# Performance work log

Hardware: AMD Instinct MI355X
Metric: run time of the kernel (lower is better)

Reference implementation:

```python
import jax, jax.numpy as jnp
import numpy as np

CODE_NUM = 12288
GRAPH = 128      # graph_size: embedding width / GRU input
HIDDEN = 128     # GRU hidden = t_output_size = time_size (required by scatter/broadcast)
ATT = 64         # t_attention_size


def setup_inputs() -> dict:
    key = jax.random.key(0)
    ks = jax.random.split(key, 20)
    s = 0.05
    # disjoint 3-way membership masks (m1/m2/m3), some codes in no set
    cat = jax.random.randint(ks[0], (CODE_NUM,), 0, 4)
    divided = jax.nn.one_hot(cat, 4, dtype=jnp.int32)[:, :3]
    return {
        "interval": jnp.asarray(3.5, jnp.float32),
        "co_embeddings": jax.random.normal(ks[1], (CODE_NUM, GRAPH), jnp.float32),
        "no_embeddings": jax.random.normal(ks[2], (CODE_NUM, GRAPH), jnp.float32),
        "unrelated_embeddings": jax.random.normal(ks[3], (CODE_NUM, GRAPH), jnp.float32),
        "hidden_state": jax.random.normal(ks[4], (CODE_NUM, HIDDEN), jnp.float32),
        "divided": divided,
        # GRUCell params (torch layout: [3H, in], gates r|z|n)
        "W_ih": jax.random.normal(ks[5], (3 * HIDDEN, GRAPH), jnp.float32) * s,
        "W_hh": jax.random.normal(ks[6], (3 * HIDDEN, HIDDEN), jnp.float32) * s,
        "b_ih": jax.random.normal(ks[7], (3 * HIDDEN,), jnp.float32) * s,
        "b_hh": jax.random.normal(ks[8], (3 * HIDDEN,), jnp.float32) * s,
        # SingleHeadAttentionLayer params
        "Wq": jax.random.normal(ks[9], (ATT, GRAPH), jnp.float32) * s,
        "bq": jax.random.normal(ks[10], (ATT,), jnp.float32) * s,
        "Wk": jax.random.normal(ks[11], (ATT, GRAPH), jnp.float32) * s,
        "bk": jax.random.normal(ks[12], (ATT,), jnp.float32) * s,
        "Wv": jax.random.normal(ks[13], (HIDDEN, GRAPH), jnp.float32) * s,
        "bv": jax.random.normal(ks[14], (HIDDEN,), jnp.float32) * s,
        # time_layer: Linear(1, time_size)
        "Wt": jax.random.normal(ks[15], (HIDDEN, 1), jnp.float32) * s,
        "bt": jax.random.normal(ks[16], (HIDDEN,), jnp.float32) * s,
        "t": 1,
        "is_last": 0,
    }


def _gru_cell(x, h, W_ih, W_hh, b_ih, b_hh):
    gi = x @ W_ih.T + b_ih          # [N, 3H]
    gh = h @ W_hh.T + b_hh          # [N, 3H]
    i_r, i_z, i_n = jnp.split(gi, 3, axis=-1)
    h_r, h_z, h_n = jnp.split(gh, 3, axis=-1)
    r = jax.nn.sigmoid(i_r + h_r)
    z = jax.nn.sigmoid(i_z + h_z)
    n = jnp.tanh(i_n + r * h_n)
    return (1.0 - z) * n + z * h


def reference(interval, co_embeddings, no_embeddings, unrelated_embeddings,
              hidden_state, divided, W_ih, W_hh, b_ih, b_hh,
              Wq, bq, Wk, bk, Wv, bv, Wt, bt, t, is_last):
    dt = co_embeddings.dtype
    # time feature: tanh(Linear(1/log(interval + e)))
    x_t = 1.0 / jnp.log(interval + jnp.e)                       # scalar
    time_features = jnp.tanh(x_t * Wt[:, 0] + bt)               # [H]

    if is_last:
        out = _gru_cell(co_embeddings, hidden_state, W_ih, W_hh, b_ih, b_hh)
        return (out + time_features, None)

    m1 = divided[:, 0] > 0
    m2 = divided[:, 1] > 0
    m3 = divided[:, 2] > 0
    m23 = m2 | m3
    NEG = jnp.finfo(dt).min

    # --- m1 branch: GRUCell is row-wise, so compute on all rows and mask ---
    h_gru = _gru_cell(co_embeddings, hidden_state, W_ih, W_hh, b_ih, b_hh)  # [N, H]
    output_m1 = jnp.max(jnp.where(m1[:, None], h_gru, NEG), axis=0)        # [H]

    # --- m2/m3 branch: attention over the m23 subset (mask-based, order-free)
    # query rows: m2 -> no_embeddings, m3 -> unrelated_embeddings
    q_full = jnp.where(m2[:, None], no_embeddings, unrelated_embeddings)   # [N, G]
    Q = q_full @ Wq.T + bq                                                 # [N, A]
    K = co_embeddings @ Wk.T + bk                                          # [N, A]
    V = co_embeddings @ Wv.T + bv                                          # [N, H]
    scores = (Q @ K.T) / jnp.sqrt(jnp.asarray(ATT, dt))                    # [N, N]
    scores = jnp.where(m23[None, :], scores, NEG)                          # keys restricted to m23
    attn = jax.nn.softmax(scores, axis=-1)
    h_att = jnp.tanh(attn @ V)                                             # [N, H]
    output_m23 = jnp.max(jnp.where(m23[:, None], h_att, NEG), axis=0)      # [H]

    # scatter: m2/m3 rows written after m1 rows (m23 takes precedence)
    h_new = jnp.where(m23[:, None], h_att,
                      jnp.where(m1[:, None], h_gru, jnp.zeros((), dt)))

    output = jnp.maximum(output_m1, output_m23)
    return (output + time_features, h_new)
```

## Files before the change

### kernel.cpp

```cpp
#include <hip/hip_runtime.h>
#include <hip/hip_bf16.h>
#include <math.h>

#define N_CODES 12288
#define G 128
#define H 128
#define ATT 64
#define NEGF (-3.4028234663852886e38f)
#define NSEG 8
#define QT 64
#define QMAX 7168
#define NQTA (QMAX / QT)

typedef __attribute__((ext_vector_type(8))) short bf16x8;
typedef __attribute__((ext_vector_type(4))) float f32x4;
typedef __hip_bfloat16 bf16;
#define MFMA16(a, b, c) __builtin_amdgcn_mfma_f32_16x16x32_bf16(a, b, c, 0, 0, 0)

struct __align__(16) Ws {
  int n1;
  int n23;
  int cnt;
  int pad_;
  int idx1[N_CODES];
  int rows23[N_CODES];
  int flags23[N_CODES];
  unsigned maxu[128];
  float tf[128];
  float lseg[NSEG * QMAX];
  float bqkv[256];
  float b2[512];
  bf16 Wqkv[16 * 4 * 64 * 8];
  bf16 W2[32 * 8 * 64 * 8];
  bf16 Qb[(size_t)N_CODES * ATT];
  bf16 Kf[(size_t)N_CODES * ATT];
  bf16 Vf[(size_t)N_CODES * H];
  bf16 Oseg[(size_t)NSEG * QMAX * H];
};

__device__ inline uint2 pack4(float4 v) {
  union { bf16 b[4]; uint2 u; } cv;
  cv.b[0] = __float2bfloat16(v.x);
  cv.b[1] = __float2bfloat16(v.y);
  cv.b[2] = __float2bfloat16(v.z);
  cv.b[3] = __float2bfloat16(v.w);
  return cv.u;
}

__device__ inline float bf2f(short s) {
  union { unsigned u; float f; } c;
  c.u = ((unsigned)(unsigned short)s) << 16;
  return c.f;
}

__device__ inline unsigned fkey(float f) {
  unsigned b = __float_as_uint(f);
  return (b & 0x80000000u) ? ~b : (b | 0x80000000u);
}
__device__ inline float funkey(unsigned u) {
  unsigned b = (u & 0x80000000u) ? (u & 0x7fffffffu) : ~u;
  return __uint_as_float(b);
}

__global__ void k_setup(const int* __restrict__ divided,
                        const float* __restrict__ Wq, const float* __restrict__ bq,
                        const float* __restrict__ Wk, const float* __restrict__ bk,
                        const float* __restrict__ Wv, const float* __restrict__ bv,
                        const float* __restrict__ W_ih, const float* __restrict__ W_hh,
                        const float* __restrict__ b_ih, const float* __restrict__ b_hh,
                        const float* __restrict__ interval, const float* __restrict__ Wt,
                        const float* __restrict__ bt, Ws* ws, float* __restrict__ h_new) {
  int bid = blockIdx.x;
  int t = threadIdx.x;
  if (bid < 48) {
    int r = bid * 256 + t;
    int m1 = divided[r * 3 + 0] > 0;
    int m2 = divided[r * 3 + 1] > 0;
    int m3 = divided[r * 3 + 2] > 0;
    if (m1) {
      int p = atomicAdd(&ws->n1, 1);
      ws->idx1[p] = r;
    }
    if (m2 | m3) {
      int p = atomicAdd(&ws->n23, 1);
      ws->rows23[p] = r;
      ws->flags23[p] = m2;
    }
    if (!(m1 | m2 | m3)) {
      float4 z = {0.f, 0.f, 0.f, 0.f};
      float4* hr = (float4*)&h_new[(size_t)r * H];
#pragma unroll
      for (int i = 0; i < 32; ++i) hr[i] = z;
    }
    return;
  }
  if (bid < 80) {
    int idx = (bid - 48) * 256 + t;
    int c = idx >> 5, k = (idx & 31) * 4;
    float4 v;
    if (c < 64) {
      v = *(const float4*)&Wq[c * G + k];
      v.x *= 0.125f; v.y *= 0.125f; v.z *= 0.125f; v.w *= 0.125f;
    } else if (c < 128) {
      v = *(const float4*)&Wk[(c - 64) * G + k];
    } else {
      v = *(const float4*)&Wv[(c - 128) * G + k];
    }
    int NB = c >> 4, lo = c & 15, ks = k >> 5, hi = (k >> 3) & 3, j = k & 7;
    *(uint2*)&ws->Wqkv[((NB * 4 + ks) * 64 + hi * 16 + lo) * 8 + j] = pack4(v);
    return;
  }
  if (bid < 208) {
    int idx = (bid - 80) * 256 + t;
    int c = idx >> 6, k = (idx & 63) * 4;
    int g = c >> 7, d = c & 127;
    float4 v = {0.f, 0.f, 0.f, 0.f};
    if (g == 0) v = (k < 128) ? *(const float4*)&W_ih[d * G + k]
                              : *(const float4*)&W_hh[d * H + (k - 128)];
    else if (g == 1) v = (k < 128) ? *(const float4*)&W_ih[(128 + d) * G + k]
                                   : *(const float4*)&W_hh[(128 + d) * H + (k - 128)];
    else if (g == 2) { if (k < 128) v = *(const float4*)&W_ih[(256 + d) * G + k]; }
    else { if (k >= 128) v = *(const float4*)&W_hh[(256 + d) * H + (k - 128)]; }
    int NB = c >> 4, lo = c & 15, ks = k >> 5, hi = (k >> 3) & 3, j = k & 7;
    *(uint2*)&ws->W2[((NB * 8 + ks) * 64 + hi * 16 + lo) * 8 + j] = pack4(v);
    return;
  }
  if (t < 128) {
    float xt = 1.0f / logf(interval[0] + 2.718281828459045f);
    ws->tf[t] = tanhf(xt * Wt[t] + bt[t]);
    ws->maxu[t] = 0u;
  }
  for (int i = t; i < 768; i += 256) {
    if (i < 256) {
      float v;
      if (i < 64) v = bq[i] * 0.125f;
      else if (i < 128) v = bk[i - 64];
      else v = bv[i - 128];
      ws->bqkv[i] = v;
    } else {
      int c = i - 256;
      int g = c >> 7, d = c & 127;
      float v;
      if (g == 0) v = b_ih[d] + b_hh[d];
      else if (g == 1) v = b_ih[128 + d] + b_hh[128 + d];
      else if (g == 2) v = b_ih[256 + d];
      else v = b_hh[256 + d];
      ws->b2[c] = v;
    }
  }
}

__launch_bounds__(256)
__global__ void k_mm(const float* __restrict__ co, const float* __restrict__ no_e,
                     const float* __restrict__ un_e, const float* __restrict__ hs,
                     Ws* ws, float* __restrict__ h_new) {
  __shared__ __align__(16) bf16 sm[8704];
  int bid = blockIdx.x;
  int t = threadIdx.x;
  int w = t >> 6, lane = t & 63, lo = lane & 15, hi = lane >> 4;

  if (bid < 448) {
    int n23 = ws->n23;
    int q0 = bid * 16;
    if (q0 >= n23) return;
    bf16(*Aq)[136] = (bf16(*)[136])sm;
    bf16(*Ac)[136] = (bf16(*)[136])(sm + 2176);
    for (int it = 0; it < 2; ++it) {
      int idx = it * 256 + t;
      int rr = idx >> 5, c4 = idx & 31;
      uint2 pq = {0, 0}, pc = {0, 0};
      int p = q0 + rr;
      if (p < n23) {
        int row = ws->rows23[p];
        const float* srcq = ws->flags23[p] ? no_e : un_e;
        pq = pack4(*(const float4*)&srcq[(size_t)row * G + c4 * 4]);
        pc = pack4(*(const float4*)&co[(size_t)row * G + c4 * 4]);
      }
      *(uint2*)&Aq[rr][c4 * 4] = pq;
      *(uint2*)&Ac[rr][c4 * 4] = pc;
    }
    __syncthreads();
    const bf16(*At)[136] = (w == 0) ? Aq : Ac;
    f32x4 acc[4];
#pragma unroll
    for (int nb = 0; nb < 4; ++nb) acc[nb] = (f32x4){0.f, 0.f, 0.f, 0.f};
#pragma unroll
    for (int ks = 0; ks < 4; ++ks) {
      bf16x8 af = *(const bf16x8*)&At[lo][ks * 32 + hi * 8];
#pragma unroll
      for (int nb = 0; nb < 4; ++nb) {
        bf16x8 bfr = *(const bf16x8*)&ws->Wqkv[(((w * 4 + nb) * 4 + ks) * 64 + lane) * 8];
        acc[nb] = MFMA16(af, bfr, acc[nb]);
      }
    }
#pragma unroll
    for (int nb = 0; nb < 4; ++nb) {
      int c = w * 64 + nb * 16 + lo;
      float bias = ws->bqkv[c];
#pragma unroll
      for (int r = 0; r < 4; ++r) {
        int p = q0 + hi * 4 + r;
        if (p >= n23) continue;
        bf16 bv16 = __float2bfloat16(acc[nb][r] + bias);
        if (c < 64) {
          ws->Qb[(size_t)p * ATT + c] = bv16;
        } else if (c < 128) {
          int d = c - 64;
          ws->Kf[(((p >> 4) * 2 + (d >> 5)) * 64 + ((d >> 3) & 3) * 16 + (p & 15)) * 8 + (d & 7)] = bv16;
        } else {
          int d = c - 128;
          ws->Vf[((((p >> 6) * 8 + (d >> 4)) * 2 + ((p >> 5) & 1)) * 64 + ((p >> 3) & 3) * 16 + (d & 15)) * 8 + (p & 7)] = bv16;
        }
      }
    }
  } else {
    int n1 = ws->n1;
    int q0 = (bid - 448) * 16;
    if (q0 >= n1) return;
    bf16(*A2)[264] = (bf16(*)[264])sm;
    for (int it = 0; it < 4; ++it) {
      int idx = it * 256 + t;
      int rr = idx >> 6, c4 = idx & 63;
      uint2 pk = {0, 0};
      int p = q0 + rr;
      if (p < n1) {
        int row = ws->idx1[p];
        float4 v = (c4 < 32) ? *(const float4*)&co[(size_t)row * G + c4 * 4]
                             : *(const float4*)&hs[(size_t)row * H + (c4 - 32) * 4];
        pk = pack4(v);
      }
      *(uint2*)&A2[rr][c4 * 4] = pk;
    }
    __syncthreads();
    f32x4 acc[8];
#pragma unroll
    for (int x = 0; x < 8; ++x) acc[x] = (f32x4){0.f, 0.f, 0.f, 0.f};
#pragma unroll
    for (int ks = 0; ks < 8; ++ks) {
      bf16x8 af = *(const bf16x8*)&A2[lo][ks * 32 + hi * 8];
#pragma unroll
      for (int g = 0; g < 4; ++g) {
#pragma unroll
        for (int nb2 = 0; nb2 < 2; ++nb2) {
          int NB = g * 8 + w * 2 + nb2;
          bf16x8 bfr = *(const bf16x8*)&ws->W2[((NB * 8 + ks) * 64 + lane) * 8];
          acc[g * 2 + nb2] = MFMA16(af, bfr, acc[g * 2 + nb2]);
        }
      }
    }
    float mx2[2] = {NEGF, NEGF};
#pragma unroll
    for (int nb2 = 0; nb2 < 2; ++nb2) {
      int d = w * 32 + nb2 * 16 + lo;
      float br = ws->b2[d], bz = ws->b2[128 + d], bin_ = ws->b2[256 + d], bhn = ws->b2[384 + d];
#pragma unroll
      for (int r = 0; r < 4; ++r) {
        int p = q0 + hi * 4 + r;
        if (p >= n1) continue;
        int row = ws->idx1[p];
        float rs = acc[0 + nb2][r] + br;
        float zs = acc[2 + nb2][r] + bz;
        float in_ = acc[4 + nb2][r] + bin_;
        float hn = acc[6 + nb2][r] + bhn;
        float rg = 1.f / (1.f + __expf(-rs));
        float zg = 1.f / (1.f + __expf(-zs));
        float ng = tanhf(in_ + rg * hn);
        float h0 = hs[(size_t)row * H + d];
        float hv = (1.f - zg) * ng + zg * h0;
        h_new[(size_t)row * H + d] = hv;
        mx2[nb2] = fmaxf(mx2[nb2], hv);
      }
    }
#pragma unroll
    for (int nb2 = 0; nb2 < 2; ++nb2) {
      float m = mx2[nb2];
      m = fmaxf(m, __shfl_xor(m, 16));
      m = fmaxf(m, __shfl_xor(m, 32));
      if (hi == 0) atomicMax(&ws->maxu[w * 32 + nb2 * 16 + lo], fkey(m));
    }
  }
}

__launch_bounds__(256)
__global__ void k_attn(const Ws* __restrict__ ws, Ws* __restrict__ wso) {
  int n23 = ws->n23;
  int bid = blockIdx.x;
  int q0 = (bid % NQTA) * QT;
  int seg = bid / NQTA;
  if (q0 >= n23) return;
  int segk = (((n23 + NSEG - 1) / NSEG) + 63) & ~63;
  int s0 = seg * segk;
  int t = threadIdx.x;
  if (s0 >= n23) {
    for (int idx = t; idx < QT * 32; idx += 256) {
      int q = q0 + (idx >> 5);
      if (q < n23) {
        uint2 z2 = {0, 0};
        *(uint2*)&wso->Oseg[((size_t)seg * QMAX + q) * H + (idx & 31) * 4] = z2;
      }
    }
    if (t < QT && q0 + t < n23) wso->lseg[seg * QMAX + q0 + t] = 0.f;
    return;
  }
  int send = min(s0 + segk, n23);

  int w = t >> 6, lane = t & 63, lo = lane & 15, hi = lane >> 4;

  __shared__ bf16 Pl[64][72];
  __shared__ float Lw[4][64];

  bf16x8 qf[4][2];
#pragma unroll
  for (int qsub = 0; qsub < 4; ++qsub)
#pragma unroll
    for (int s = 0; s < 2; ++s)
      qf[qsub][s] =
          *(const bf16x8*)&ws->Qb[(size_t)(q0 + qsub * 16 + lo) * ATT + s * 32 + hi * 8];

  f32x4 acc[2][4];
#pragma unroll
  for (int ddl = 0; ddl < 2; ++ddl)
#pragma unroll
    for (int qsub = 0; qsub < 4; ++qsub) acc[ddl][qsub] = (f32x4){0.f, 0.f, 0.f, 0.f};
  float lacc[4] = {0.f, 0.f, 0.f, 0.f};

  for (int c0 = s0; c0 < send; c0 += 64) {
    int kb = (c0 >> 4) + w;
    bf16x8 kf0 = *(const bf16x8*)&ws->Kf[((size_t)(kb * 2 + 0) * 64 + lane) * 8];
    bf16x8 kf1 = *(const bf16x8*)&ws->Kf[((size_t)(kb * 2 + 1) * 64 + lane) * 8];
#pragma unroll
    for (int qsub = 0; qsub < 4; ++qsub) {
      f32x4 s_ = {0.f, 0.f, 0.f, 0.f};
      s_ = MFMA16(kf0, qf[qsub][0], s_);
      s_ = MFMA16(kf1, qf[qsub][1], s_);
      union { bf16 b[4]; uint2 u; } tu;
      float sl = 0.f;
#pragma unroll
      for (int r = 0; r < 4; ++r) {
        int key = c0 + w * 16 + hi * 4 + r;
        float p = (key < send) ? __expf(s_[r]) : 0.f;
        sl += p;
        tu.b[r] = __float2bfloat16(p);
      }
      *(uint2*)&Pl[qsub * 16 + lo][w * 16 + hi * 4] = tu.u;
      sl += __shfl_xor(sl, 16);
      sl += __shfl_xor(sl, 32);
      lacc[qsub] += sl;
    }
    __syncthreads();

    int kc = c0 >> 6;
    bf16x8 vf[2][2];
#pragma unroll
    for (int s = 0; s < 2; ++s)
#pragma unroll
      for (int ddl = 0; ddl < 2; ++ddl)
        vf[s][ddl] =
            *(const bf16x8*)&ws->Vf[((size_t)(kc * 16 + (w * 2 + ddl) * 2 + s) * 64 + lane) * 8];
#pragma unroll
    for (int s = 0; s < 2; ++s) {
      bf16x8 pf[4];
#pragma unroll
      for (int qsub = 0; qsub < 4; ++qsub)
        pf[qsub] = *(const bf16x8*)&Pl[qsub * 16 + lo][s * 32 + hi * 8];
#pragma unroll
      for (int ddl = 0; ddl < 2; ++ddl)
#pragma unroll
        for (int qsub = 0; qsub < 4; ++qsub)
          acc[ddl][qsub] = MFMA16(vf[s][ddl], pf[qsub], acc[ddl][qsub]);
    }
    __syncthreads();
  }

  if (hi == 0) {
#pragma unroll
    for (int qsub = 0; qsub < 4; ++qsub) Lw[w][qsub * 16 + lo] = lacc[qsub];
  }
  __syncthreads();
  if (t < QT) {
    int q = q0 + t;
    if (q < n23) wso->lseg[seg * QMAX + q] = Lw[0][t] + Lw[1][t] + Lw[2][t] + Lw[3][t];
  }
#pragma unroll
  for (int qsub = 0; qsub < 4; ++qsub) {
    int q = q0 + qsub * 16 + lo;
    if (q < n23) {
#pragma unroll
      for (int ddl = 0; ddl < 2; ++ddl) {
        union { bf16 b[4]; uint2 u; } tmp;
#pragma unroll
        for (int r = 0; r < 4; ++r) tmp.b[r] = __float2bfloat16(acc[ddl][qsub][r]);
        *(uint2*)&wso->Oseg[((size_t)seg * QMAX + q) * H + w * 32 + ddl * 16 + hi * 4] = tmp.u;
      }
    }
  }
}

__global__ void k_merge(const Ws* __restrict__ ws, float* __restrict__ h_new, Ws* wso,
                        float* __restrict__ out) {
  int n23 = ws->n23;
  int qb = blockIdx.x * 16;
  if (qb >= n23) return;
  int t = threadIdx.x;
  int ql = t >> 4, d8 = (t & 15) * 8;
  int q = qb + ql;

  __shared__ float red[16][128];
  float h8[8];
  bool act = q < n23;
  if (act) {
    float o[8];
#pragma unroll
    for (int j = 0; j < 8; ++j) o[j] = 0.f;
    float L = 0.f;
#pragma unroll
    for (int s = 0; s < NSEG; ++s) {
      bf16x8 ov = *(const bf16x8*)&ws->Oseg[((size_t)s * QMAX + q) * H + d8];
#pragma unroll
      for (int j = 0; j < 8; ++j) o[j] += bf2f(ov[j]);
      L += ws->lseg[s * QMAX + q];
    }
    float linv = 1.0f / L;
    float4 h0, h1;
#pragma unroll
    for (int j = 0; j < 8; ++j) h8[j] = tanhf(o[j] * linv);
    h0.x = h8[0]; h0.y = h8[1]; h0.z = h8[2]; h0.w = h8[3];
    h1.x = h8[4]; h1.y = h8[5]; h1.z = h8[6]; h1.w = h8[7];
    float* hr = &h_new[(size_t)ws->rows23[q] * H + d8];
    *(float4*)hr = h0;
    *(float4*)(hr + 4) = h1;
  } else {
#pragma unroll
    for (int j = 0; j < 8; ++j) h8[j] = NEGF;
  }
#pragma unroll
  for (int j = 0; j < 8; ++j) red[ql][d8 + j] = h8[j];
  __syncthreads();
  if (t < 128) {
    float m = NEGF;
#pragma unroll
    for (int ql2 = 0; ql2 < 16; ++ql2) m = fmaxf(m, red[ql2][t]);
    atomicMax(&wso->maxu[t], fkey(m));
  }
  __shared__ int lastv;
  __syncthreads();
  if (t == 0) {
    __threadfence();
    int nact = (n23 + 15) >> 4;
    lastv = (atomicAdd(&wso->cnt, 1) == nact - 1) ? 1 : 0;
  }
  __syncthreads();
  if (lastv && t < 128) {
    unsigned u = atomicOr(&wso->maxu[t], 0u);
    out[t] = funkey(u) + ws->tf[t];
  }
}

extern "C" void kernel_launch(void* const* d_in, const int* in_sizes, int n_in,
                              void* d_out, int out_size, void* d_ws, size_t ws_size,
                              hipStream_t stream) {
  const float* interval = (const float*)d_in[0];
  const float* co = (const float*)d_in[1];
  const float* no_e = (const float*)d_in[2];
  const float* un_e = (const float*)d_in[3];
  const float* hs = (const float*)d_in[4];
  const int* divided = (const int*)d_in[5];
  const float* W_ih = (const float*)d_in[6];
  const float* W_hh = (const float*)d_in[7];
  const float* b_ih = (const float*)d_in[8];
  const float* b_hh = (const float*)d_in[9];
  const float* Wq = (const float*)d_in[10];
  const float* bq = (const float*)d_in[11];
  const float* Wk = (const float*)d_in[12];
  const float* bk = (const float*)d_in[13];
  const float* Wv = (const float*)d_in[14];
  const float* bv = (const float*)d_in[15];
  const float* Wt = (const float*)d_in[16];
  const float* bt = (const float*)d_in[17];

  float* out = (float*)d_out;
  float* h_new = out + 128;
  Ws* ws = (Ws*)d_ws;

  hipMemsetAsync(ws, 0, 16, stream);

  k_setup<<<209, 256, 0, stream>>>(divided, Wq, bq, Wk, bk, Wv, bv, W_ih, W_hh, b_ih, b_hh,
                                   interval, Wt, bt, ws, h_new);
  k_mm<<<704, 256, 0, stream>>>(co, no_e, un_e, hs, ws, h_new);
  k_attn<<<NQTA * NSEG, 256, 0, stream>>>(ws, ws);
  k_merge<<<(QMAX + 15) / 16, 256, 0, stream>>>(ws, h_new, ws, out);
}
```

Before: 182.8 us.

## Split projection/GRU blocks in half by output columns and shrink attention query tile

```diff
diff --git a/kernel.cpp b/kernel.cpp
--- a/kernel.cpp
+++ b/kernel.cpp
@@ -8,7 +8,7 @@
 #define ATT 64
 #define NEGF (-3.4028234663852886e38f)
 #define NSEG 8
-#define QT 64
+#define QT 32
 #define QMAX 7168
 #define NQTA (QMAX / QT)
 
@@ -159,9 +159,10 @@
   int t = threadIdx.x;
   int w = t >> 6, lane = t & 63, lo = lane & 15, hi = lane >> 4;
 
-  if (bid < 448) {
+  if (bid < 768) {
     int n23 = ws->n23;
-    int q0 = bid * 16;
+    int q0 = (bid >> 1) * 16;
+    int z = bid & 1;
     if (q0 >= n23) return;
     bf16(*Aq)[136] = (bf16(*)[136])sm;
     bf16(*Ac)[136] = (bf16(*)[136])(sm + 2176);
@@ -172,30 +173,33 @@
       int p = q0 + rr;
       if (p < n23) {
         int row = ws->rows23[p];
-        const float* srcq = ws->flags23[p] ? no_e : un_e;
-        pq = pack4(*(const float4*)&srcq[(size_t)row * G + c4 * 4]);
         pc = pack4(*(const float4*)&co[(size_t)row * G + c4 * 4]);
-      }
-      *(uint2*)&Aq[rr][c4 * 4] = pq;
+        if (z == 0) {
+          const float* srcq = ws->flags23[p] ? no_e : un_e;
+          pq = pack4(*(const float4*)&srcq[(size_t)row * G + c4 * 4]);
+        }
+      }
+      if (z == 0) *(uint2*)&Aq[rr][c4 * 4] = pq;
       *(uint2*)&Ac[rr][c4 * 4] = pc;
     }
     __syncthreads();
-    const bf16(*At)[136] = (w == 0) ? Aq : Ac;
-    f32x4 acc[4];
-#pragma unroll
-    for (int nb = 0; nb < 4; ++nb) acc[nb] = (f32x4){0.f, 0.f, 0.f, 0.f};
+    const bf16(*At)[136] = (z == 0 && w < 2) ? Aq : Ac;
+    f32x4 acc[2];
+#pragma unroll
+    for (int nb = 0; nb < 2; ++nb) acc[nb] = (f32x4){0.f, 0.f, 0.f, 0.f};
 #pragma unroll
     for (int ks = 0; ks < 4; ++ks) {
       bf16x8 af = *(const bf16x8*)&At[lo][ks * 32 + hi * 8];
 #pragma unroll
-      for (int nb = 0; nb < 4; ++nb) {
-        bf16x8 bfr = *(const bf16x8*)&ws->Wqkv[(((w * 4 + nb) * 4 + ks) * 64 + lane) * 8];
+      for (int nb = 0; nb < 2; ++nb) {
+        int NBg = z * 8 + w * 2 + nb;
+        bf16x8 bfr = *(const bf16x8*)&ws->Wqkv[((NBg * 4 + ks) * 64 + lane) * 8];
         acc[nb] = MFMA16(af, bfr, acc[nb]);
       }
     }
 #pragma unroll
-    for (int nb = 0; nb < 4; ++nb) {
-      int c = w * 64 + nb * 16 + lo;
+    for (int nb = 0; nb < 2; ++nb) {
+      int c = z * 128 + w * 32 + nb * 16 + lo;
       float bias = ws->bqkv[c];
 #pragma unroll
       for (int r = 0; r < 4; ++r) {
@@ -215,7 +219,8 @@
     }
   } else {
     int n1 = ws->n1;
-    int q0 = (bid - 448) * 16;
+    int q0 = ((bid - 768) >> 1) * 16;
+    int z = bid & 1;
     if (q0 >= n1) return;
     bf16(*A2)[264] = (bf16(*)[264])sm;
     for (int it = 0; it < 4; ++it) {
@@ -232,52 +237,42 @@
       *(uint2*)&A2[rr][c4 * 4] = pk;
     }
     __syncthreads();
-    f32x4 acc[8];
-#pragma unroll
-    for (int x = 0; x < 8; ++x) acc[x] = (f32x4){0.f, 0.f, 0.f, 0.f};
+    f32x4 acc[4];
+#pragma unroll
+    for (int g = 0; g < 4; ++g) acc[g] = (f32x4){0.f, 0.f, 0.f, 0.f};
 #pragma unroll
     for (int ks = 0; ks < 8; ++ks) {
       bf16x8 af = *(const bf16x8*)&A2[lo][ks * 32 + hi * 8];
 #pragma unroll
       for (int g = 0; g < 4; ++g) {
-#pragma unroll
-        for (int nb2 = 0; nb2 < 2; ++nb2) {
-          int NB = g * 8 + w * 2 + nb2;
-          bf16x8 bfr = *(const bf16x8*)&ws->W2[((NB * 8 + ks) * 64 + lane) * 8];
-          acc[g * 2 + nb2] = MFMA16(af, bfr, acc[g * 2 + nb2]);
-        }
-      }
-    }
-    float mx2[2] = {NEGF, NEGF};
-#pragma unroll
-    for (int nb2 = 0; nb2 < 2; ++nb2) {
-      int d = w * 32 + nb2 * 16 + lo;
-      float br = ws->b2[d], bz = ws->b2[128 + d], bin_ = ws->b2[256 + d], bhn = ws->b2[384 + d];
-#pragma unroll
-      for (int r = 0; r < 4; ++r) {
-        int p = q0 + hi * 4 + r;
-        if (p >= n1) continue;
-        int row = ws->idx1[p];
-        float rs = acc[0 + nb2][r] + br;
-        float zs = acc[2 + nb2][r] + bz;
-        float in_ = acc[4 + nb2][r] + bin_;
-        float hn = acc[6 + nb2][r] + bhn;
-        float rg = 1.f / (1.f + __expf(-rs));
-        float zg = 1.f / (1.f + __expf(-zs));
-        float ng = tanhf(in_ + rg * hn);
-        float h0 = hs[(size_t)row * H + d];
-        float hv = (1.f - zg) * ng + zg * h0;
-        h_new[(size_t)row * H + d] = hv;
-        mx2[nb2] = fmaxf(mx2[nb2], hv);
-      }
-    }
-#pragma unroll
-    for (int nb2 = 0; nb2 < 2; ++nb2) {
-      float m = mx2[nb2];
-      m = fmaxf(m, __shfl_xor(m, 16));
-      m = fmaxf(m, __shfl_xor(m, 32));
-      if (hi == 0) atomicMax(&ws->maxu[w * 32 + nb2 * 16 + lo], fkey(m));
-    }
+        int NB = g * 8 + z * 4 + w;
+        bf16x8 bfr = *(const bf16x8*)&ws->W2[((NB * 8 + ks) * 64 + lane) * 8];
+        acc[g] = MFMA16(af, bfr, acc[g]);
+      }
+    }
+    int d = z * 64 + w * 16 + lo;
+    float br = ws->b2[d], bz = ws->b2[128 + d], bin_ = ws->b2[256 + d], bhn = ws->b2[384 + d];
+    float mx = NEGF;
+#pragma unroll
+    for (int r = 0; r < 4; ++r) {
+      int p = q0 + hi * 4 + r;
+      if (p >= n1) continue;
+      int row = ws->idx1[p];
+      float rs = acc[0][r] + br;
+      float zs = acc[1][r] + bz;
+      float in_ = acc[2][r] + bin_;
+      float hn = acc[3][r] + bhn;
+      float rg = 1.f / (1.f + __expf(-rs));
+      float zg = 1.f / (1.f + __expf(-zs));
+      float ng = tanhf(in_ + rg * hn);
+      float h0 = hs[(size_t)row * H + d];
+      float hv = (1.f - zg) * ng + zg * h0;
+      h_new[(size_t)row * H + d] = hv;
+      mx = fmaxf(mx, hv);
+    }
+    mx = fmaxf(mx, __shfl_xor(mx, 16));
+    mx = fmaxf(mx, __shfl_xor(mx, 32));
+    if (hi == 0) atomicMax(&ws->maxu[d], fkey(mx));
   }
 }
 
@@ -306,30 +301,30 @@
 
   int w = t >> 6, lane = t & 63, lo = lane & 15, hi = lane >> 4;
 
-  __shared__ bf16 Pl[64][72];
-  __shared__ float Lw[4][64];
-
-  bf16x8 qf[4][2];
-#pragma unroll
-  for (int qsub = 0; qsub < 4; ++qsub)
+  __shared__ bf16 Pl[32][72];
+  __shared__ float Lw[4][32];
+
+  bf16x8 qf[2][2];
+#pragma unroll
+  for (int qsub = 0; qsub < 2; ++qsub)
 #pragma unroll
     for (int s = 0; s < 2; ++s)
       qf[qsub][s] =
           *(const bf16x8*)&ws->Qb[(size_t)(q0 + qsub * 16 + lo) * ATT + s * 32 + hi * 8];
 
-  f32x4 acc[2][4];
+  f32x4 acc[2][2];
 #pragma unroll
   for (int ddl = 0; ddl < 2; ++ddl)
 #pragma unroll
-    for (int qsub = 0; qsub < 4; ++qsub) acc[ddl][qsub] = (f32x4){0.f, 0.f, 0.f, 0.f};
-  float lacc[4] = {0.f, 0.f, 0.f, 0.f};
+    for (int qsub = 0; qsub < 2; ++qsub) acc[ddl][qsub] = (f32x4){0.f, 0.f, 0.f, 0.f};
+  float lacc[2] = {0.f, 0.f};
 
   for (int c0 = s0; c0 < send; c0 += 64) {
     int kb = (c0 >> 4) + w;
     bf16x8 kf0 = *(const bf16x8*)&ws->Kf[((size_t)(kb * 2 + 0) * 64 + lane) * 8];
     bf16x8 kf1 = *(const bf16x8*)&ws->Kf[((size_t)(kb * 2 + 1) * 64 + lane) * 8];
 #pragma unroll
-    for (int qsub = 0; qsub < 4; ++qsub) {
+    for (int qsub = 0; qsub < 2; ++qsub) {
       f32x4 s_ = {0.f, 0.f, 0.f, 0.f};
       s_ = MFMA16(kf0, qf[qsub][0], s_);
       s_ = MFMA16(kf1, qf[qsub][1], s_);
@@ -359,14 +354,14 @@
             *(const bf16x8*)&ws->Vf[((size_t)(kc * 16 + (w * 2 + ddl) * 2 + s) * 64 + lane) * 8];
 #pragma unroll
     for (int s = 0; s < 2; ++s) {
-      bf16x8 pf[4];
-#pragma unroll
-      for (int qsub = 0; qsub < 4; ++qsub)
+      bf16x8 pf[2];
+#pragma unroll
+      for (int qsub = 0; qsub < 2; ++qsub)
         pf[qsub] = *(const bf16x8*)&Pl[qsub * 16 + lo][s * 32 + hi * 8];
 #pragma unroll
       for (int ddl = 0; ddl < 2; ++ddl)
 #pragma unroll
-        for (int qsub = 0; qsub < 4; ++qsub)
+        for (int qsub = 0; qsub < 2; ++qsub)
           acc[ddl][qsub] = MFMA16(vf[s][ddl], pf[qsub], acc[ddl][qsub]);
     }
     __syncthreads();
@@ -374,7 +369,7 @@
 
   if (hi == 0) {
 #pragma unroll
-    for (int qsub = 0; qsub < 4; ++qsub) Lw[w][qsub * 16 + lo] = lacc[qsub];
+    for (int qsub = 0; qsub < 2; ++qsub) Lw[w][qsub * 16 + lo] = lacc[qsub];
   }
   __syncthreads();
   if (t < QT) {
@@ -382,7 +377,7 @@
     if (q < n23) wso->lseg[seg * QMAX + q] = Lw[0][t] + Lw[1][t] + Lw[2][t] + Lw[3][t];
   }
 #pragma unroll
-  for (int qsub = 0; qsub < 4; ++qsub) {
+  for (int qsub = 0; qsub < 2; ++qsub) {
     int q = q0 + qsub * 16 + lo;
     if (q < n23) {
 #pragma unroll
@@ -486,7 +481,7 @@
 
   k_setup<<<209, 256, 0, stream>>>(divided, Wq, bq, Wk, bk, Wv, bv, W_ih, W_hh, b_ih, b_hh,
                                    interval, Wt, bt, ws, h_new);
-  k_mm<<<704, 256, 0, stream>>>(co, no_e, un_e, hs, ws, h_new);
+  k_mm<<<1536, 256, 0, stream>>>(co, no_e, un_e, hs, ws, h_new);
   k_attn<<<NQTA * NSEG, 256, 0, stream>>>(ws, ws);
   k_merge<<<(QMAX + 15) / 16, 256, 0, stream>>>(ws, h_new, ws, out);
 }
```

After: 180.2 us (median of 2 runs). Within noise of the previous version (-1.4%).
